# Kernel optimization log

Hardware: AMD Instinct MI355X
Metric: run time of the kernel (lower is better)

The kernel has to match this reference:

```python
import jax, jax.numpy as jnp
import numpy as np

B, L, D = 4, 2048, 128  # batch, input_dim == seq_len, memory/key/query/value dim
EPS_RMS = float(np.finfo(np.float32).eps)  # torch nn.RMSNorm default eps
EPS_NORM = 1e-12                           # F.normalize default eps


def setup_inputs() -> dict:
    key = jax.random.key(0)
    ks = jax.random.split(key, 20)
    s = 0.02
    rnd = lambda k, shape: jax.random.normal(k, shape, jnp.float32) * s
    return {
        "x": jax.random.normal(ks[0], (B, L, L), jnp.float32),
        "k_proj_w": rnd(ks[1], (D, L)), "k_proj_b": rnd(ks[2], (D,)),
        "q_proj_w": rnd(ks[3], (D, L)), "q_proj_b": rnd(ks[4], (D,)),
        "v_proj_w": rnd(ks[5], (D, L)), "v_proj_b": rnd(ks[6], (D,)),
        "k_conv_w": rnd(ks[7], (D, D, 3, 3)), "k_conv_b": rnd(ks[8], (D,)),
        "q_conv_w": rnd(ks[9], (D, D, 3, 3)), "q_conv_b": rnd(ks[10], (D,)),
        "v_conv_w": rnd(ks[11], (D, D, 3, 3)), "v_conv_b": rnd(ks[12], (D,)),
        "beta_w": rnd(ks[13], (1, L)), "beta_b": rnd(ks[14], (1,)),
        "rms_w": jnp.ones((D,), jnp.float32),
        "out_w": rnd(ks[15], (L, D)), "out_b": rnd(ks[16], (L,)),
    }


def _conv3x3(x4, w, b):
    # x4: (B, Cin, H, 1); w: (Cout, Cin, 3, 3); padding=1 both dims (torch Conv2d)
    y = jax.lax.conv_general_dilated(
        x4, w, window_strides=(1, 1), padding=((1, 1), (1, 1)),
        dimension_numbers=("NCHW", "OIHW", "NCHW"))
    return y + b[None, :, None, None]


def _l2_normalize_last(x):
    # F.normalize(p=2, dim=-1): here last dim is the SEQUENCE dim (faithful to source)
    n = jnp.sqrt(jnp.sum(x * x, axis=-1, keepdims=True))
    return x / jnp.maximum(n, EPS_NORM)


def _delta_rule(k, q, v, beta):
    # k, q, v: (B, D, L); beta: (B, L, 1)
    # S_t = S_{t-1} (I - b_t k_t k_t^T) + b_t v_t k_t^T ; o_t = S_t q_t
    kt = jnp.transpose(k, (2, 0, 1))          # (L, B, D)
    qt = jnp.transpose(q, (2, 0, 1))
    vt = jnp.transpose(v, (2, 0, 1))
    bt = jnp.transpose(beta, (1, 0, 2))       # (L, B, 1)

    S0 = jnp.zeros((k.shape[0], k.shape[1], k.shape[1]), k.dtype)

    def step(S, xs):
        k_t, q_t, v_t, b_t = xs               # (B,D),(B,D),(B,D),(B,1)
        b = b_t[:, :, None]                   # (B,1,1)
        Sk = jnp.einsum("bij,bj->bi", S, k_t)  # (B,D)
        S = S - b * (Sk[:, :, None] * k_t[:, None, :]) \
              + b * (v_t[:, :, None] * k_t[:, None, :])
        o = jnp.einsum("bij,bj->bi", S, q_t)   # (B,D)
        return S, o

    _, o = jax.lax.scan(step, S0, (kt, qt, vt, bt))
    return jnp.transpose(o, (1, 0, 2))        # (B, L, D)


def reference(x, k_proj_w, k_proj_b, q_proj_w, q_proj_b, v_proj_w, v_proj_b,
              k_conv_w, k_conv_b, q_conv_w, q_conv_b, v_conv_w, v_conv_b,
              beta_w, beta_b, rms_w, out_w, out_b):
    b_, _, sl = x.shape                       # (B, L, L); seq_len == input_dim
    k = x @ k_proj_w.T + k_proj_b             # (B, L, D)
    q = x @ q_proj_w.T + q_proj_b
    v = x @ v_proj_w.T + v_proj_b
    # torch .view on contiguous tensor = raw row-major reshape (NOT transpose)
    k = k.reshape(b_, D, sl, 1)
    q = q.reshape(b_, D, sl, 1)
    v = v.reshape(b_, D, sl, 1)
    k = _conv3x3(k, k_conv_w, k_conv_b).reshape(b_, D, sl)
    q = _conv3x3(q, q_conv_w, q_conv_b).reshape(b_, D, sl)
    v = _conv3x3(v, v_conv_w, v_conv_b).reshape(b_, D, sl)
    k, q, v = jax.nn.silu(k), jax.nn.silu(q), jax.nn.silu(v)
    k, q = _l2_normalize_last(k), _l2_normalize_last(q)
    beta = jax.nn.sigmoid(x @ beta_w.T + beta_b)      # (B, L, 1)
    delta = _delta_rule(k, q, v, beta)                # (B, L, D)
    # RMSNorm over memory_dim (last axis), affine weight
    ms = jnp.mean(delta * delta, axis=-1, keepdims=True)
    normed = delta * jax.lax.rsqrt(ms + EPS_RMS) * rms_w
    return normed @ out_w.T + out_b                   # (B, L, input_dim)
```

## Files before the change

### kernel.cpp

```cpp
#include <hip/hip_runtime.h>
#include <math.h>

#define LL 2048
#define DD 128
#define BB 4
#define CK 64
#define NCHUNK 32

typedef __bf16 bf16x8 __attribute__((ext_vector_type(8)));
typedef __bf16 bf16x4 __attribute__((ext_vector_type(4)));
typedef float floatx4 __attribute__((ext_vector_type(4)));

__global__ __launch_bounds__(256) void proj_gemm_mfma(
    const float* __restrict__ x,
    const float* __restrict__ kw, const float* __restrict__ qw, const float* __restrict__ vw,
    const float* __restrict__ kb, const float* __restrict__ qb, const float* __restrict__ vb,
    float* __restrict__ k0, float* __restrict__ q0, float* __restrict__ v0)
{
    const int arr = blockIdx.y;
    const float* __restrict__ w   = arr == 0 ? kw : (arr == 1 ? qw : vw);
    const float* __restrict__ bia = arr == 0 ? kb : (arr == 1 ? qb : vb);
    float* __restrict__ out       = arr == 0 ? k0 : (arr == 1 ? q0 : v0);

    __shared__ __bf16 As[128][72];
    __shared__ __bf16 Bs[128][72];

    const int t    = threadIdx.x;
    const int wave = t >> 6, lane = t & 63;
    const int wm   = wave & 1, wn = wave >> 1;
    const int m    = lane & 15, quad = lane >> 4;
    const int row0 = blockIdx.x * 128;

    floatx4 acc[4][4] = {};

    for (int k0i = 0; k0i < 2048; k0i += 64) {
        #pragma unroll
        for (int c = 0; c < 4; c++) {
            int chunk = t + c * 256;
            int r = chunk >> 3, p = chunk & 7;
            const float4* src = (const float4*)&x[(size_t)(row0 + r) * 2048 + k0i + p * 8];
            float4 f0 = src[0], f1 = src[1];
            bf16x8 v8;
            v8[0] = (__bf16)f0.x; v8[1] = (__bf16)f0.y; v8[2] = (__bf16)f0.z; v8[3] = (__bf16)f0.w;
            v8[4] = (__bf16)f1.x; v8[5] = (__bf16)f1.y; v8[6] = (__bf16)f1.z; v8[7] = (__bf16)f1.w;
            *(bf16x8*)&As[r][p * 8] = v8;
        }
        #pragma unroll
        for (int c = 0; c < 4; c++) {
            int chunk = t + c * 256;
            int r = chunk >> 3, p = chunk & 7;
            const float4* src = (const float4*)&w[(size_t)r * 2048 + k0i + p * 8];
            float4 f0 = src[0], f1 = src[1];
            bf16x8 v8;
            v8[0] = (__bf16)f0.x; v8[1] = (__bf16)f0.y; v8[2] = (__bf16)f0.z; v8[3] = (__bf16)f0.w;
            v8[4] = (__bf16)f1.x; v8[5] = (__bf16)f1.y; v8[6] = (__bf16)f1.z; v8[7] = (__bf16)f1.w;
            *(bf16x8*)&Bs[r][p * 8] = v8;
        }
        __syncthreads();
        #pragma unroll
        for (int ks = 0; ks < 2; ks++) {
            bf16x8 af[4], bfr[4];
            #pragma unroll
            for (int i = 0; i < 4; i++)
                af[i] = *(const bf16x8*)&As[wm * 64 + i * 16 + m][ks * 32 + quad * 8];
            #pragma unroll
            for (int j = 0; j < 4; j++)
                bfr[j] = *(const bf16x8*)&Bs[wn * 64 + j * 16 + m][ks * 32 + quad * 8];
            #pragma unroll
            for (int i = 0; i < 4; i++)
                #pragma unroll
                for (int j = 0; j < 4; j++)
                    acc[i][j] = __builtin_amdgcn_mfma_f32_16x16x32_bf16(af[i], bfr[j], acc[i][j], 0, 0, 0);
        }
        __syncthreads();
    }
    #pragma unroll
    for (int i = 0; i < 4; i++) {
        int grow = row0 + wm * 64 + i * 16 + quad * 4;
        #pragma unroll
        for (int j = 0; j < 4; j++) {
            int col = wn * 64 + j * 16 + m;
            float bv = bia[col];
            #pragma unroll
            for (int r = 0; r < 4; r++)
                out[(size_t)(grow + r) * 128 + col] = acc[i][j][r] + bv;
        }
    }
}

__global__ __launch_bounds__(256) void out_gemm_mfma(
    const __bf16* __restrict__ A, const float* __restrict__ w,
    const float* __restrict__ bias, float* __restrict__ out)
{
    __shared__ __bf16 As[128][72];
    __shared__ __bf16 Bs[128][72];

    const int t    = threadIdx.x;
    const int wave = t >> 6, lane = t & 63;
    const int wm   = wave & 1, wn = wave >> 1;
    const int m    = lane & 15, quad = lane >> 4;
    const int row0 = blockIdx.x * 128;
    const int col0 = blockIdx.y * 128;

    floatx4 acc[4][4] = {};

    for (int k0i = 0; k0i < 128; k0i += 64) {
        #pragma unroll
        for (int c = 0; c < 4; c++) {
            int chunk = t + c * 256;
            int r = chunk >> 3, p = chunk & 7;
            *(bf16x8*)&As[r][p * 8] = *(const bf16x8*)&A[(size_t)(row0 + r) * 128 + k0i + p * 8];
        }
        #pragma unroll
        for (int c = 0; c < 4; c++) {
            int chunk = t + c * 256;
            int r = chunk >> 3, p = chunk & 7;
            const float4* src = (const float4*)&w[(size_t)(col0 + r) * 128 + k0i + p * 8];
            float4 f0 = src[0], f1 = src[1];
            bf16x8 v8;
            v8[0] = (__bf16)f0.x; v8[1] = (__bf16)f0.y; v8[2] = (__bf16)f0.z; v8[3] = (__bf16)f0.w;
            v8[4] = (__bf16)f1.x; v8[5] = (__bf16)f1.y; v8[6] = (__bf16)f1.z; v8[7] = (__bf16)f1.w;
            *(bf16x8*)&Bs[r][p * 8] = v8;
        }
        __syncthreads();
        #pragma unroll
        for (int ks = 0; ks < 2; ks++) {
            bf16x8 af[4], bfr[4];
            #pragma unroll
            for (int i = 0; i < 4; i++)
                af[i] = *(const bf16x8*)&As[wm * 64 + i * 16 + m][ks * 32 + quad * 8];
            #pragma unroll
            for (int j = 0; j < 4; j++)
                bfr[j] = *(const bf16x8*)&Bs[wn * 64 + j * 16 + m][ks * 32 + quad * 8];
            #pragma unroll
            for (int i = 0; i < 4; i++)
                #pragma unroll
                for (int j = 0; j < 4; j++)
                    acc[i][j] = __builtin_amdgcn_mfma_f32_16x16x32_bf16(af[i], bfr[j], acc[i][j], 0, 0, 0);
        }
        __syncthreads();
    }
    #pragma unroll
    for (int i = 0; i < 4; i++) {
        int grow = row0 + wm * 64 + i * 16 + quad * 4;
        #pragma unroll
        for (int j = 0; j < 4; j++) {
            int col = col0 + wn * 64 + j * 16 + m;
            float bv = bias[col];
            #pragma unroll
            for (int r = 0; r < 4; r++)
                out[(size_t)(grow + r) * 2048 + col] = acc[i][j][r] + bv;
        }
    }
}

__global__ __launch_bounds__(256) void beta_kernel(
    const float* __restrict__ x, const float* __restrict__ bw,
    const float* __restrict__ bb, float* __restrict__ beta)
{
    const int row = blockIdx.x;
    const float* xr = x + (size_t)row * 2048;
    float s = 0.f;
    for (int j = threadIdx.x; j < 2048; j += 256) s = fmaf(xr[j], bw[j], s);
    #pragma unroll
    for (int m = 1; m < 64; m <<= 1) s += __shfl_xor(s, m, 64);
    __shared__ float red[4];
    if ((threadIdx.x & 63) == 0) red[threadIdx.x >> 6] = s;
    __syncthreads();
    if (threadIdx.x == 0) {
        float tot = red[0] + red[1] + red[2] + red[3] + bb[0];
        beta[row] = 1.f / (1.f + expf(-tot));
    }
}

__global__ __launch_bounds__(256) void wpack_zero(
    const float* __restrict__ kw, const float* __restrict__ qw, const float* __restrict__ vw,
    __bf16* __restrict__ wpk, float* __restrict__ sumsq)
{
    const int t = threadIdx.x;
    if (blockIdx.x == 0) {
        #pragma unroll
        for (int e = 0; e < 4; e++) sumsq[t * 4 + e] = 0.f;
    }
    int base = (blockIdx.x * 256 + t) * 4;
    int arr = base / 49152, rem = base % 49152;
    const float* __restrict__ w = arr == 0 ? kw : arr == 1 ? qw : vw;
    int dt = rem / 16384, rem2 = rem % 16384;
    int o = rem2 >> 7, i0 = rem2 & 127;
    #pragma unroll
    for (int e = 0; e < 4; e++) {
        int i = i0 + e;
        wpk[base + e] = (__bf16)w[(size_t)((o * 128 + i) * 3 + dt) * 3 + 1];
    }
}

__global__ __launch_bounds__(256) void conv_mfma(
    const float* __restrict__ k0, const float* __restrict__ q0, const float* __restrict__ v0,
    const __bf16* __restrict__ wpk,
    const float* __restrict__ kb, const float* __restrict__ qb, const float* __restrict__ vb,
    float* __restrict__ kcT, float* __restrict__ qcT, float* __restrict__ vcT,
    float* __restrict__ sumsq)
{
    const int sb  = blockIdx.x;
    const int arr = blockIdx.y >> 2;
    const int b   = blockIdx.y & 3;
    const float* __restrict__ in = (arr == 0 ? k0 : arr == 1 ? q0 : v0) + (size_t)b * DD * LL;
    const float* __restrict__ bi = arr == 0 ? kb : arr == 1 ? qb : vb;
    float* __restrict__ out      = (arr == 0 ? kcT : arr == 1 ? qcT : vcT) + (size_t)b * LL * DD;
    const __bf16* __restrict__ wp = wpk + (size_t)arr * 3 * DD * DD;

    __shared__ __bf16 Xs[66 * 136];
    __shared__ float colsum[128];

    const int t = threadIdx.x;
    const int s0 = sb * 64;
    if (t < 128) colsum[t] = 0.f;

    #pragma unroll
    for (int p = 0; p < 32; p++) {
        int idx = t + p * 256;
        int sr = idx & 63, i = idx >> 6;
        float v = in[(size_t)i * LL + s0 + sr];
        int row = sr + 1;
        Xs[row * 136 + (i ^ ((row & 7) << 4))] = (__bf16)v;
    }
    {
        int e = t >> 7, i = t & 127;
        int row = e * 65;
        int s = s0 - 1 + e * 65;
        float v = (s >= 0 && s < LL) ? in[(size_t)i * LL + s] : 0.f;
        Xs[row * 136 + (i ^ ((row & 7) << 4))] = (__bf16)v;
    }
    __syncthreads();

    const int wave = t >> 6, lane = t & 63;
    const int wm = wave & 1, wn = wave >> 1;
    const int m = lane & 15, quad = lane >> 4;

    floatx4 acc[2][4] = {};
    #pragma unroll
    for (int dt = 0; dt < 3; dt++) {
        bf16x8 bfr[4][4];
        #pragma unroll
        for (int ks = 0; ks < 4; ks++)
            #pragma unroll
            for (int j = 0; j < 4; j++)
                bfr[ks][j] = *(const bf16x8*)&wp[(size_t)(dt * DD + wn * 64 + j * 16 + m) * DD + ks * 32 + quad * 8];
        #pragma unroll
        for (int ks = 0; ks < 4; ks++) {
            bf16x8 af[2];
            #pragma unroll
            for (int ii = 0; ii < 2; ii++) {
                int row = wm * 32 + ii * 16 + m + dt;
                af[ii] = *(const bf16x8*)&Xs[row * 136 + ((ks * 32 + quad * 8) ^ ((row & 7) << 4))];
            }
            #pragma unroll
            for (int ii = 0; ii < 2; ii++)
                #pragma unroll
                for (int j = 0; j < 4; j++)
                    acc[ii][j] = __builtin_amdgcn_mfma_f32_16x16x32_bf16(af[ii], bfr[ks][j], acc[ii][j], 0, 0, 0);
        }
    }

    float part[4] = {0.f, 0.f, 0.f, 0.f};
    #pragma unroll
    for (int ii = 0; ii < 2; ii++)
        #pragma unroll
        for (int j = 0; j < 4; j++) {
            int col = wn * 64 + j * 16 + m;
            float bv = bi[col];
            #pragma unroll
            for (int r = 0; r < 4; r++) {
                int srow = s0 + wm * 32 + ii * 16 + quad * 4 + r;
                float v = acc[ii][j][r] + bv;
                float y = v / (1.f + expf(-v));
                out[(size_t)srow * DD + col] = y;
                part[j] = fmaf(y, y, part[j]);
            }
        }
    if (arr < 2) {
        #pragma unroll
        for (int j = 0; j < 4; j++)
            atomicAdd(&colsum[wn * 64 + j * 16 + m], part[j]);
        __syncthreads();
        if (t < 128) atomicAdd(&sumsq[arr * 512 + b * 128 + t], colsum[t]);
    }
}


__global__ __launch_bounds__(256) void chunk_pre1(
    const float* __restrict__ kTg, const float* __restrict__ qTg, const float* __restrict__ vTg,
    const float* __restrict__ beta, const float* __restrict__ sumsq,
    __bf16* __restrict__ Lb, __bf16* __restrict__ Wb, __bf16* __restrict__ Ub)
{
    const int c = blockIdx.x, b = blockIdx.y;
    const int gc = b * NCHUNK + c;
    const int t0 = c * CK;
    const float* kbase = kTg + ((size_t)b * LL + t0) * DD;
    const float* qbase = qTg + ((size_t)b * LL + t0) * DD;
    const float* vbase = vTg + ((size_t)b * LL + t0) * DD;

    __shared__ __bf16 Ks[CK][136];
    __shared__ __bf16 Qs[CK][136];
    __shared__ float  Af[CK][65];
    __shared__ float  WU[CK][257];
    __shared__ float  betas[CK];

    const int t = threadIdx.x;
    #pragma unroll
    for (int p = 0; p < 8; p++) {
        int idx = t + p * 256;
        int r = idx >> 5, c4 = idx & 31;
        float4 sk = *(const float4*)&sumsq[b * 128 + c4 * 4];
        float4 sq = *(const float4*)&sumsq[512 + b * 128 + c4 * 4];
        float ik0 = rsqrtf(fmaxf(sk.x, 1e-24f)), ik1 = rsqrtf(fmaxf(sk.y, 1e-24f));
        float ik2 = rsqrtf(fmaxf(sk.z, 1e-24f)), ik3 = rsqrtf(fmaxf(sk.w, 1e-24f));
        float iq0 = rsqrtf(fmaxf(sq.x, 1e-24f)), iq1 = rsqrtf(fmaxf(sq.y, 1e-24f));
        float iq2 = rsqrtf(fmaxf(sq.z, 1e-24f)), iq3 = rsqrtf(fmaxf(sq.w, 1e-24f));
        float4 f = *(const float4*)&kbase[(size_t)r * DD + c4 * 4];
        bf16x4 v; v[0] = (__bf16)(f.x * ik0); v[1] = (__bf16)(f.y * ik1);
        v[2] = (__bf16)(f.z * ik2); v[3] = (__bf16)(f.w * ik3);
        *(bf16x4*)&Ks[r][c4 * 4] = v;
        float4 g = *(const float4*)&qbase[(size_t)r * DD + c4 * 4];
        bf16x4 u; u[0] = (__bf16)(g.x * iq0); u[1] = (__bf16)(g.y * iq1);
        u[2] = (__bf16)(g.z * iq2); u[3] = (__bf16)(g.w * iq3);
        *(bf16x4*)&Qs[r][c4 * 4] = u;
    }
    if (t < CK) betas[t] = beta[(size_t)b * LL + t0 + t];
    __syncthreads();

    const int wave = t >> 6, lane = t & 63;
    const int wm = wave & 1, wn = wave >> 1;
    const int m = lane & 15, quad = lane >> 4;

    floatx4 accM[2][2] = {}, accL[2][2] = {};
    #pragma unroll
    for (int ks = 0; ks < 4; ks++) {
        bf16x8 ak[2], aq[2], bk[2];
        #pragma unroll
        for (int i = 0; i < 2; i++) {
            ak[i] = *(const bf16x8*)&Ks[wm * 32 + i * 16 + m][ks * 32 + quad * 8];
            aq[i] = *(const bf16x8*)&Qs[wm * 32 + i * 16 + m][ks * 32 + quad * 8];
            bk[i] = *(const bf16x8*)&Ks[wn * 32 + i * 16 + m][ks * 32 + quad * 8];
        }
        #pragma unroll
        for (int i = 0; i < 2; i++)
            #pragma unroll
            for (int j = 0; j < 2; j++) {
                accM[i][j] = __builtin_amdgcn_mfma_f32_16x16x32_bf16(ak[i], bk[j], accM[i][j], 0, 0, 0);
                accL[i][j] = __builtin_amdgcn_mfma_f32_16x16x32_bf16(aq[i], bk[j], accL[i][j], 0, 0, 0);
            }
    }
    #pragma unroll
    for (int i = 0; i < 2; i++)
        #pragma unroll
        for (int j = 0; j < 2; j++)
            #pragma unroll
            for (int r = 0; r < 4; r++) {
                int row = wm * 32 + i * 16 + quad * 4 + r;
                int col = wn * 32 + j * 16 + m;
                Af[row][col] = (col < row) ? betas[row] * accM[i][j][r] : 0.f;
                Lb[((size_t)gc * CK + row) * CK + col] =
                    (col <= row) ? (__bf16)accL[i][j][r] : (__bf16)0.f;
            }
    __syncthreads();

    const int col = t;
    const float* rbase = (col < DD) ? kbase : vbase;
    const int cm = col & (DD - 1);
    const float scale = (col < DD) ? rsqrtf(fmaxf(sumsq[b * 128 + cm], 1e-24f)) : 1.f;
    float cur = rbase[cm] * scale;
    for (int tt = 0; tt < CK; tt++) {
        float nxt = (tt < CK - 1) ? rbase[(size_t)(tt + 1) * DD + cm] * scale : 0.f;
        float acc = betas[tt] * cur;
        for (int s = 0; s < tt; s++)
            acc -= Af[tt][s] * WU[s][col];
        WU[tt][col] = acc;
        __bf16 bv = (__bf16)acc;
        if (col < DD) Wb[((size_t)gc * CK + tt) * DD + col] = bv;
        else          Ub[((size_t)gc * CK + tt) * DD + cm]  = bv;
        cur = nxt;
    }
}

__global__ __launch_bounds__(256) void chunk_pre2(
    const float* __restrict__ kTg, const float* __restrict__ qTg,
    const float* __restrict__ sumsq,
    const __bf16* __restrict__ Lb, const __bf16* __restrict__ Wb, const __bf16* __restrict__ Ub,
    __bf16* __restrict__ HTb, __bf16* __restrict__ Gb,
    __bf16* __restrict__ Pb, __bf16* __restrict__ Yb)
{
    const int c = blockIdx.x, b = blockIdx.y;
    const int gc = b * NCHUNK + c;
    const int t0 = c * CK;

    __shared__ __bf16 Kt[DD][72];
    __shared__ __bf16 Wt[DD][72];
    __shared__ __bf16 Ut[DD][72];
    __shared__ __bf16 Ls[CK][72];

    const int t = threadIdx.x;
    #pragma unroll
    for (int p = 0; p < 8; p++) {
        int idx = t + p * 256;
        int tt = idx >> 5, j4 = idx & 31;
        float4 sk = *(const float4*)&sumsq[b * 128 + j4 * 4];
        float4 f = *(const float4*)&kTg[((size_t)b * LL + t0 + tt) * DD + j4 * 4];
        Kt[j4 * 4 + 0][tt] = (__bf16)(f.x * rsqrtf(fmaxf(sk.x, 1e-24f)));
        Kt[j4 * 4 + 1][tt] = (__bf16)(f.y * rsqrtf(fmaxf(sk.y, 1e-24f)));
        Kt[j4 * 4 + 2][tt] = (__bf16)(f.z * rsqrtf(fmaxf(sk.z, 1e-24f)));
        Kt[j4 * 4 + 3][tt] = (__bf16)(f.w * rsqrtf(fmaxf(sk.w, 1e-24f)));
        bf16x4 w = *(const bf16x4*)&Wb[((size_t)gc * CK + tt) * DD + j4 * 4];
        bf16x4 u = *(const bf16x4*)&Ub[((size_t)gc * CK + tt) * DD + j4 * 4];
        #pragma unroll
        for (int e = 0; e < 4; e++) { Wt[j4 * 4 + e][tt] = w[e]; Ut[j4 * 4 + e][tt] = u[e]; }
    }
    #pragma unroll
    for (int p = 0; p < 4; p++) {
        int idx = t + p * 256;
        int tt = idx >> 4, s4 = idx & 15;
        *(bf16x4*)&Ls[tt][s4 * 4] = *(const bf16x4*)&Lb[((size_t)gc * CK + tt) * CK + s4 * 4];
    }
    __syncthreads();

    const int wave = t >> 6, lane = t & 63;
    const int wm = wave & 1, wn = wave >> 1;
    const int m = lane & 15, quad = lane >> 4;

    {
        floatx4 acc[4][4] = {};
        #pragma unroll
        for (int ks = 0; ks < 2; ks++) {
            bf16x8 a[4], bb[4];
            #pragma unroll
            for (int i = 0; i < 4; i++) {
                a[i]  = *(const bf16x8*)&Kt[wm * 64 + i * 16 + m][ks * 32 + quad * 8];
                bb[i] = *(const bf16x8*)&Wt[wn * 64 + i * 16 + m][ks * 32 + quad * 8];
            }
            #pragma unroll
            for (int i = 0; i < 4; i++)
                #pragma unroll
                for (int j = 0; j < 4; j++)
                    acc[i][j] = __builtin_amdgcn_mfma_f32_16x16x32_bf16(a[i], bb[j], acc[i][j], 0, 0, 0);
        }
        #pragma unroll
        for (int i = 0; i < 4; i++)
            #pragma unroll
            for (int j = 0; j < 4; j++)
                #pragma unroll
                for (int r = 0; r < 4; r++) {
                    int row = wm * 64 + i * 16 + quad * 4 + r;
                    int cx  = wn * 64 + j * 16 + m;
                    HTb[((size_t)gc * DD + row) * DD + cx] = (__bf16)(-acc[i][j][r]);
                }
    }
    {
        floatx4 acc[4][4] = {};
        #pragma unroll
        for (int ks = 0; ks < 2; ks++) {
            bf16x8 a[4], bb[4];
            #pragma unroll
            for (int i = 0; i < 4; i++) {
                a[i]  = *(const bf16x8*)&Ut[wm * 64 + i * 16 + m][ks * 32 + quad * 8];
                bb[i] = *(const bf16x8*)&Kt[wn * 64 + i * 16 + m][ks * 32 + quad * 8];
            }
            #pragma unroll
            for (int i = 0; i < 4; i++)
                #pragma unroll
                for (int j = 0; j < 4; j++)
                    acc[i][j] = __builtin_amdgcn_mfma_f32_16x16x32_bf16(a[i], bb[j], acc[i][j], 0, 0, 0);
        }
        #pragma unroll
        for (int i = 0; i < 4; i++)
            #pragma unroll
            for (int j = 0; j < 4; j++)
                #pragma unroll
                for (int r = 0; r < 4; r++) {
                    int row = wm * 64 + i * 16 + quad * 4 + r;
                    int cx  = wn * 64 + j * 16 + m;
                    Gb[((size_t)gc * DD + row) * DD + cx] = (__bf16)acc[i][j][r];
                }
    }
    {
        floatx4 acc[2][4] = {};
        #pragma unroll
        for (int ks = 0; ks < 2; ks++) {
            bf16x8 a[2], bb[4];
            #pragma unroll
            for (int i = 0; i < 2; i++)
                a[i] = *(const bf16x8*)&Ls[wm * 32 + i * 16 + m][ks * 32 + quad * 8];
            #pragma unroll
            for (int j = 0; j < 4; j++)
                bb[j] = *(const bf16x8*)&Wt[wn * 64 + j * 16 + m][ks * 32 + quad * 8];
            #pragma unroll
            for (int i = 0; i < 2; i++)
                #pragma unroll
                for (int j = 0; j < 4; j++)
                    acc[i][j] = __builtin_amdgcn_mfma_f32_16x16x32_bf16(a[i], bb[j], acc[i][j], 0, 0, 0);
        }
        #pragma unroll
        for (int i = 0; i < 2; i++)
            #pragma unroll
            for (int j = 0; j < 4; j++)
                #pragma unroll
                for (int r = 0; r < 4; r++) {
                    int row = wm * 32 + i * 16 + quad * 4 + r;
                    int cx  = wn * 64 + j * 16 + m;
                    float iq = rsqrtf(fmaxf(sumsq[512 + b * 128 + cx], 1e-24f));
                    float qv = qTg[((size_t)b * LL + t0 + row) * DD + cx] * iq;
                    Pb[((size_t)gc * CK + row) * DD + cx] = (__bf16)(qv - acc[i][j][r]);
                }
    }
    {
        floatx4 acc[2][4] = {};
        #pragma unroll
        for (int ks = 0; ks < 2; ks++) {
            bf16x8 a[2], bb[4];
            #pragma unroll
            for (int i = 0; i < 2; i++)
                a[i] = *(const bf16x8*)&Ls[wm * 32 + i * 16 + m][ks * 32 + quad * 8];
            #pragma unroll
            for (int j = 0; j < 4; j++)
                bb[j] = *(const bf16x8*)&Ut[wn * 64 + j * 16 + m][ks * 32 + quad * 8];
            #pragma unroll
            for (int i = 0; i < 2; i++)
                #pragma unroll
                for (int j = 0; j < 4; j++)
                    acc[i][j] = __builtin_amdgcn_mfma_f32_16x16x32_bf16(a[i], bb[j], acc[i][j], 0, 0, 0);
        }
        #pragma unroll
        for (int i = 0; i < 2; i++)
            #pragma unroll
            for (int j = 0; j < 4; j++)
                #pragma unroll
                for (int r = 0; r < 4; r++) {
                    int row = wm * 32 + i * 16 + quad * 4 + r;
                    int cx  = wn * 64 + j * 16 + m;
                    Yb[((size_t)gc * CK + row) * DD + cx] = (__bf16)acc[i][j][r];
                }
    }
}

__global__ __launch_bounds__(256) void delta_serial(
    const __bf16* __restrict__ HTb, const __bf16* __restrict__ Gb, __bf16* __restrict__ S0b)
{
    const int b  = blockIdx.x >> 2;
    const int rg = blockIdx.x & 3;
    __shared__ __bf16 Ss[32][136];
    const int t = threadIdx.x;
    const int wj = t >> 6;
    const int lane = t & 63;
    const int m = lane & 15, quad = lane >> 4;

    floatx4 acc[2][2] = {};
    bf16x8 hA[8], hB[8];
    __bf16 gpre[16];

    {
        const size_t g0 = (size_t)(b * NCHUNK) * DD * DD;
        #pragma unroll
        for (int ks = 0; ks < 4; ks++)
            #pragma unroll
            for (int j = 0; j < 2; j++) {
                int hr = wj * 32 + j * 16 + m;
                hA[ks * 2 + j] = *(const bf16x8*)&HTb[g0 + (size_t)hr * DD + ks * 32 + quad * 8];
            }
        #pragma unroll
        for (int i = 0; i < 2; i++)
            #pragma unroll
            for (int j = 0; j < 2; j++)
                #pragma unroll
                for (int r = 0; r < 4; r++) {
                    int row = rg * 32 + i * 16 + quad * 4 + r;
                    int cx  = wj * 32 + j * 16 + m;
                    gpre[(i * 2 + j) * 4 + r] = Gb[g0 + (size_t)row * DD + cx];
                }
    }

    for (int c = 0; c < NCHUNK; c++) {
        const size_t gco = (size_t)(b * NCHUNK + c) * DD * DD;
        const size_t gcn = gco + (size_t)DD * DD;
        const bool even = (c & 1) == 0;
        if (c + 1 < NCHUNK) {
            #pragma unroll
            for (int ks = 0; ks < 4; ks++)
                #pragma unroll
                for (int j = 0; j < 2; j++) {
                    int hr = wj * 32 + j * 16 + m;
                    bf16x8 v = *(const bf16x8*)&HTb[gcn + (size_t)hr * DD + ks * 32 + quad * 8];
                    if (even) hB[ks * 2 + j] = v; else hA[ks * 2 + j] = v;
                }
        }
        #pragma unroll
        for (int i = 0; i < 2; i++)
            #pragma unroll
            for (int j = 0; j < 2; j++) {
                int row = i * 16 + quad * 4;
                int cx  = wj * 32 + j * 16 + m;
                #pragma unroll
                for (int r = 0; r < 4; r++)
                    Ss[row + r][cx] = (__bf16)acc[i][j][r];
            }
        __syncthreads();
        #pragma unroll
        for (int p = 0; p < 4; p++) {
            int idx = t + p * 256;
            int row = idx >> 5, c4 = idx & 31;
            *(bf16x4*)&S0b[gco + (size_t)(rg * 32 + row) * DD + c4 * 4] =
                *(const bf16x4*)&Ss[row][c4 * 4];
        }
        #pragma unroll
        for (int i = 0; i < 2; i++)
            #pragma unroll
            for (int j = 0; j < 2; j++)
                #pragma unroll
                for (int r = 0; r < 4; r++)
                    acc[i][j][r] += (float)gpre[(i * 2 + j) * 4 + r];
        if (c + 1 < NCHUNK) {
            #pragma unroll
            for (int i = 0; i < 2; i++)
                #pragma unroll
                for (int j = 0; j < 2; j++)
                    #pragma unroll
                    for (int r = 0; r < 4; r++) {
                        int row = rg * 32 + i * 16 + quad * 4 + r;
                        int cx  = wj * 32 + j * 16 + m;
                        gpre[(i * 2 + j) * 4 + r] = Gb[gcn + (size_t)row * DD + cx];
                    }
        }
        #pragma unroll
        for (int ks = 0; ks < 4; ks++) {
            bf16x8 a[2];
            #pragma unroll
            for (int i = 0; i < 2; i++)
                a[i] = *(const bf16x8*)&Ss[i * 16 + m][ks * 32 + quad * 8];
            #pragma unroll
            for (int i = 0; i < 2; i++)
                #pragma unroll
                for (int j = 0; j < 2; j++) {
                    bf16x8 hb = even ? hA[ks * 2 + j] : hB[ks * 2 + j];
                    acc[i][j] = __builtin_amdgcn_mfma_f32_16x16x32_bf16(a[i], hb, acc[i][j], 0, 0, 0);
                }
        }
        __syncthreads();
    }
}

__global__ __launch_bounds__(256) void chunk_out(
    const __bf16* __restrict__ Pb, const __bf16* __restrict__ Yb, const __bf16* __restrict__ S0b,
    const float* __restrict__ rms_w, __bf16* __restrict__ nmb)
{
    const int c = blockIdx.x, b = blockIdx.y;
    const int gc = b * NCHUNK + c;
    const int t0 = c * CK;
    __shared__ __bf16 Ps[CK][136];
    __shared__ __bf16 Sb[DD][136];
    __shared__ float red[2][2][2][4][4];
    const int t = threadIdx.x;
    #pragma unroll
    for (int p = 0; p < 8; p++) {
        int idx = t + p * 256;
        int row = idx >> 5, c4 = idx & 31;
        *(bf16x4*)&Ps[row][c4 * 4] = *(const bf16x4*)&Pb[((size_t)gc * CK + row) * DD + c4 * 4];
    }
    #pragma unroll
    for (int p = 0; p < 16; p++) {
        int idx = t + p * 256;
        int row = idx >> 5, c4 = idx & 31;
        *(bf16x4*)&Sb[row][c4 * 4] = *(const bf16x4*)&S0b[((size_t)gc * DD + row) * DD + c4 * 4];
    }
    __syncthreads();

    const int wave = t >> 6, lane = t & 63;
    const int wm = wave & 1, wn = wave >> 1;
    const int m = lane & 15, quad = lane >> 4;

    floatx4 acc[2][4] = {};
    #pragma unroll
    for (int ks = 0; ks < 4; ks++) {
        bf16x8 a[2], bb[4];
        #pragma unroll
        for (int i = 0; i < 2; i++)
            a[i] = *(const bf16x8*)&Ps[wm * 32 + i * 16 + m][ks * 32 + quad * 8];
        #pragma unroll
        for (int j = 0; j < 4; j++)
            bb[j] = *(const bf16x8*)&Sb[wn * 64 + j * 16 + m][ks * 32 + quad * 8];
        #pragma unroll
        for (int i = 0; i < 2; i++)
            #pragma unroll
            for (int j = 0; j < 4; j++)
                acc[i][j] = __builtin_amdgcn_mfma_f32_16x16x32_bf16(a[i], bb[j], acc[i][j], 0, 0, 0);
    }

    float v[2][4][4];
    float ss[2][4] = {};
    #pragma unroll
    for (int i = 0; i < 2; i++)
        #pragma unroll
        for (int j = 0; j < 4; j++)
            #pragma unroll
            for (int r = 0; r < 4; r++) {
                int row = wm * 32 + i * 16 + quad * 4 + r;
                int cx  = wn * 64 + j * 16 + m;
                float y = (float)Yb[((size_t)gc * CK + row) * DD + cx];
                float vv = acc[i][j][r] + y;
                v[i][j][r] = vv;
                ss[i][r] = fmaf(vv, vv, ss[i][r]);
            }
    #pragma unroll
    for (int mask = 1; mask < 16; mask <<= 1)
        #pragma unroll
        for (int i = 0; i < 2; i++)
            #pragma unroll
            for (int r = 0; r < 4; r++)
                ss[i][r] += __shfl_xor(ss[i][r], mask, 64);
    if (m == 0)
        #pragma unroll
        for (int i = 0; i < 2; i++)
            #pragma unroll
            for (int r = 0; r < 4; r++)
                red[wn][wm][i][quad][r] = ss[i][r];
    __syncthreads();
    #pragma unroll
    for (int i = 0; i < 2; i++)
        #pragma unroll
        for (int r = 0; r < 4; r++) {
            float tot = red[0][wm][i][quad][r] + red[1][wm][i][quad][r];
            float inv = rsqrtf(tot * (1.f / 128.f) + 1.1920928955078125e-07f);
            int row = wm * 32 + i * 16 + quad * 4 + r;
            #pragma unroll
            for (int j = 0; j < 4; j++) {
                int cx = wn * 64 + j * 16 + m;
                nmb[((size_t)b * LL + t0 + row) * DD + cx] = (__bf16)(v[i][j][r] * inv * rms_w[cx]);
            }
        }
}

extern "C" void kernel_launch(void* const* d_in, const int* in_sizes, int n_in,
                              void* d_out, int out_size, void* d_ws, size_t ws_size,
                              hipStream_t stream) {
    const float* x    = (const float*)d_in[0];
    const float* kpw  = (const float*)d_in[1];
    const float* kpb  = (const float*)d_in[2];
    const float* qpw  = (const float*)d_in[3];
    const float* qpb  = (const float*)d_in[4];
    const float* vpw  = (const float*)d_in[5];
    const float* vpb  = (const float*)d_in[6];
    const float* kcw  = (const float*)d_in[7];
    const float* kcb  = (const float*)d_in[8];
    const float* qcw  = (const float*)d_in[9];
    const float* qcb  = (const float*)d_in[10];
    const float* vcw  = (const float*)d_in[11];
    const float* vcb  = (const float*)d_in[12];
    const float* bw   = (const float*)d_in[13];
    const float* bb   = (const float*)d_in[14];
    const float* rw   = (const float*)d_in[15];
    const float* ow   = (const float*)d_in[16];
    const float* obi  = (const float*)d_in[17];
    float* out = (float*)d_out;

    float* ws = (float*)d_ws;
    const size_t NB1 = (size_t)BB * DD * LL;
    float* k0  = ws;
    float* q0  = ws + NB1;
    float* v0  = ws + 2 * NB1;
    float* kcT = ws + 3 * NB1;
    float* qcT = ws + 4 * NB1;
    float* vcT = ws + 5 * NB1;
    float* beta  = ws + 8 * NB1;
    float* sumsq = beta + (size_t)BB * LL;
    __bf16* wpk  = (__bf16*)(sumsq + 1024);

    __bf16* Lb  = (__bf16*)k0;
    __bf16* Wb  = Lb + (size_t)128 * 64 * 64;
    __bf16* Ub  = (__bf16*)q0;
    __bf16* HTb = (__bf16*)v0;
    __bf16* Gb  = (__bf16*)vcT;
    __bf16* Pb  = (__bf16*)(ws + 7 * NB1);
    __bf16* Yb  = Pb + (size_t)128 * 64 * 128;
    __bf16* S0b = (__bf16*)k0;
    __bf16* nmb = (__bf16*)(ws + 6 * NB1);

    proj_gemm_mfma<<<dim3(64, 3), 256, 0, stream>>>(x, kpw, qpw, vpw, kpb, qpb, vpb, k0, q0, v0);
    beta_kernel<<<dim3(BB * LL), 256, 0, stream>>>(x, bw, bb, beta);
    wpack_zero<<<dim3(144), 256, 0, stream>>>(kcw, qcw, vcw, wpk, sumsq);
    conv_mfma<<<dim3(32, 12), 256, 0, stream>>>(k0, q0, v0, wpk, kcb, qcb, vcb, kcT, qcT, vcT, sumsq);
    chunk_pre1<<<dim3(NCHUNK, BB), 256, 0, stream>>>(kcT, qcT, vcT, beta, sumsq, Lb, Wb, Ub);
    chunk_pre2<<<dim3(NCHUNK, BB), 256, 0, stream>>>(kcT, qcT, sumsq, Lb, Wb, Ub, HTb, Gb, Pb, Yb);
    delta_serial<<<dim3(BB * 4), 256, 0, stream>>>(HTb, Gb, S0b);
    chunk_out<<<dim3(NCHUNK, BB), 256, 0, stream>>>(Pb, Yb, S0b, rw, nmb);
    out_gemm_mfma<<<dim3(64, 16), 256, 0, stream>>>(nmb, ow, obi, out);
}
```

Before: 364.6 us.

## Pre-convert x and weights to bf16, double-buffer projection GEMM with direct-to-LDS loads

The beta kernel now also writes a bf16 copy of x into the output buffer, which serves as scratch. The weight-pack kernel converts the projection and output weights to bf16 once. The projection GEMM reads these bf16 operands with global_load_lds into double-buffered shared memory, using 64-row tiles to launch more blocks. The output GEMM loads its full K=128 tile in one pass. The aim is to remove repeated fp32-to-bf16 conversion inside the GEMM inner loops and to overlap loads with MFMA work. The cost is an extra bf16 write and read of x. The unpadded LDS layout may also cause bank conflicts.

```diff
diff --git a/kernel.cpp b/kernel.cpp
--- a/kernel.cpp
+++ b/kernel.cpp
@@ -11,63 +11,71 @@
 typedef __bf16 bf16x4 __attribute__((ext_vector_type(4)));
 typedef float floatx4 __attribute__((ext_vector_type(4)));
 
+__device__ __forceinline__ void gload_lds16(const void* g, void* l) {
+    __builtin_amdgcn_global_load_lds(
+        (const __attribute__((address_space(1))) unsigned int*)g,
+        (__attribute__((address_space(3))) unsigned int*)l, 16, 0, 0);
+}
+
 __global__ __launch_bounds__(256) void proj_gemm_mfma(
-    const float* __restrict__ x,
-    const float* __restrict__ kw, const float* __restrict__ qw, const float* __restrict__ vw,
+    const __bf16* __restrict__ xb, const __bf16* __restrict__ wcat,
     const float* __restrict__ kb, const float* __restrict__ qb, const float* __restrict__ vb,
     float* __restrict__ k0, float* __restrict__ q0, float* __restrict__ v0)
 {
     const int arr = blockIdx.y;
-    const float* __restrict__ w   = arr == 0 ? kw : (arr == 1 ? qw : vw);
     const float* __restrict__ bia = arr == 0 ? kb : (arr == 1 ? qb : vb);
     float* __restrict__ out       = arr == 0 ? k0 : (arr == 1 ? q0 : v0);
-
-    __shared__ __bf16 As[128][72];
-    __shared__ __bf16 Bs[128][72];
-
-    const int t    = threadIdx.x;
+    const __bf16* __restrict__ w  = wcat + (size_t)arr * DD * 2048;
+
+    __shared__ __bf16 As[2][64 * 64];
+    __shared__ __bf16 Bs[2][128 * 64];
+
+    const int t = threadIdx.x;
     const int wave = t >> 6, lane = t & 63;
-    const int wm   = wave & 1, wn = wave >> 1;
-    const int m    = lane & 15, quad = lane >> 4;
-    const int row0 = blockIdx.x * 128;
-
-    floatx4 acc[4][4] = {};
-
-    for (int k0i = 0; k0i < 2048; k0i += 64) {
-        #pragma unroll
-        for (int c = 0; c < 4; c++) {
-            int chunk = t + c * 256;
-            int r = chunk >> 3, p = chunk & 7;
-            const float4* src = (const float4*)&x[(size_t)(row0 + r) * 2048 + k0i + p * 8];
-            float4 f0 = src[0], f1 = src[1];
-            bf16x8 v8;
-            v8[0] = (__bf16)f0.x; v8[1] = (__bf16)f0.y; v8[2] = (__bf16)f0.z; v8[3] = (__bf16)f0.w;
-            v8[4] = (__bf16)f1.x; v8[5] = (__bf16)f1.y; v8[6] = (__bf16)f1.z; v8[7] = (__bf16)f1.w;
-            *(bf16x8*)&As[r][p * 8] = v8;
-        }
-        #pragma unroll
-        for (int c = 0; c < 4; c++) {
-            int chunk = t + c * 256;
-            int r = chunk >> 3, p = chunk & 7;
-            const float4* src = (const float4*)&w[(size_t)r * 2048 + k0i + p * 8];
-            float4 f0 = src[0], f1 = src[1];
-            bf16x8 v8;
-            v8[0] = (__bf16)f0.x; v8[1] = (__bf16)f0.y; v8[2] = (__bf16)f0.z; v8[3] = (__bf16)f0.w;
-            v8[4] = (__bf16)f1.x; v8[5] = (__bf16)f1.y; v8[6] = (__bf16)f1.z; v8[7] = (__bf16)f1.w;
-            *(bf16x8*)&Bs[r][p * 8] = v8;
-        }
-        __syncthreads();
+    const int wm = wave & 1, wn = wave >> 1;
+    const int m = lane & 15, quad = lane >> 4;
+    const int row0 = blockIdx.x * 64;
+
+    floatx4 acc[2][4] = {};
+
+    #pragma unroll
+    for (int c = 0; c < 2; c++) {
+        int f = t + c * 256;
+        gload_lds16(&xb[(size_t)(row0 + (f >> 3)) * 2048 + (f & 7) * 8], &As[0][f * 8]);
+    }
+    #pragma unroll
+    for (int c = 0; c < 4; c++) {
+        int f = t + c * 256;
+        gload_lds16(&w[(size_t)(f >> 3) * 2048 + (f & 7) * 8], &Bs[0][f * 8]);
+    }
+    __syncthreads();
+
+    for (int kt = 0; kt < 32; kt++) {
+        const int cur = kt & 1, nxt = cur ^ 1;
+        if (kt + 1 < 32) {
+            const int k0i = (kt + 1) * 64;
+            #pragma unroll
+            for (int c = 0; c < 2; c++) {
+                int f = t + c * 256;
+                gload_lds16(&xb[(size_t)(row0 + (f >> 3)) * 2048 + k0i + (f & 7) * 8], &As[nxt][f * 8]);
+            }
+            #pragma unroll
+            for (int c = 0; c < 4; c++) {
+                int f = t + c * 256;
+                gload_lds16(&w[(size_t)(f >> 3) * 2048 + k0i + (f & 7) * 8], &Bs[nxt][f * 8]);
+            }
+        }
         #pragma unroll
         for (int ks = 0; ks < 2; ks++) {
-            bf16x8 af[4], bfr[4];
-            #pragma unroll
-            for (int i = 0; i < 4; i++)
-                af[i] = *(const bf16x8*)&As[wm * 64 + i * 16 + m][ks * 32 + quad * 8];
-            #pragma unroll
-            for (int j = 0; j < 4; j++)
-                bfr[j] = *(const bf16x8*)&Bs[wn * 64 + j * 16 + m][ks * 32 + quad * 8];
-            #pragma unroll
-            for (int i = 0; i < 4; i++)
+            bf16x8 af[2], bfr[4];
+            #pragma unroll
+            for (int i = 0; i < 2; i++)
+                af[i] = *(const bf16x8*)&As[cur][(wm * 32 + i * 16 + m) * 64 + ks * 32 + quad * 8];
+            #pragma unroll
+            for (int j = 0; j < 4; j++)
+                bfr[j] = *(const bf16x8*)&Bs[cur][(wn * 64 + j * 16 + m) * 64 + ks * 32 + quad * 8];
+            #pragma unroll
+            for (int i = 0; i < 2; i++)
                 #pragma unroll
                 for (int j = 0; j < 4; j++)
                     acc[i][j] = __builtin_amdgcn_mfma_f32_16x16x32_bf16(af[i], bfr[j], acc[i][j], 0, 0, 0);
@@ -75,70 +83,54 @@
         __syncthreads();
     }
     #pragma unroll
-    for (int i = 0; i < 4; i++) {
-        int grow = row0 + wm * 64 + i * 16 + quad * 4;
+    for (int i = 0; i < 2; i++)
         #pragma unroll
         for (int j = 0; j < 4; j++) {
             int col = wn * 64 + j * 16 + m;
             float bv = bia[col];
             #pragma unroll
             for (int r = 0; r < 4; r++)
-                out[(size_t)(grow + r) * 128 + col] = acc[i][j][r] + bv;
-        }
-    }
+                out[(size_t)(row0 + wm * 32 + i * 16 + quad * 4 + r) * 128 + col] = acc[i][j][r] + bv;
+        }
 }
 
 __global__ __launch_bounds__(256) void out_gemm_mfma(
-    const __bf16* __restrict__ A, const float* __restrict__ w,
+    const __bf16* __restrict__ A, const __bf16* __restrict__ wb,
     const float* __restrict__ bias, float* __restrict__ out)
 {
-    __shared__ __bf16 As[128][72];
-    __shared__ __bf16 Bs[128][72];
-
-    const int t    = threadIdx.x;
+    __shared__ __bf16 As[128 * 128];
+    __shared__ __bf16 Bs[128 * 128];
+
+    const int t = threadIdx.x;
     const int wave = t >> 6, lane = t & 63;
-    const int wm   = wave & 1, wn = wave >> 1;
-    const int m    = lane & 15, quad = lane >> 4;
+    const int wm = wave & 1, wn = wave >> 1;
+    const int m = lane & 15, quad = lane >> 4;
     const int row0 = blockIdx.x * 128;
     const int col0 = blockIdx.y * 128;
 
+    #pragma unroll
+    for (int c = 0; c < 8; c++) {
+        int f = t + c * 256;
+        gload_lds16(&A[(size_t)(row0 + (f >> 4)) * 128 + (f & 15) * 8], &As[f * 8]);
+        gload_lds16(&wb[(size_t)(col0 + (f >> 4)) * 128 + (f & 15) * 8], &Bs[f * 8]);
+    }
+    __syncthreads();
+
     floatx4 acc[4][4] = {};
-
-    for (int k0i = 0; k0i < 128; k0i += 64) {
-        #pragma unroll
-        for (int c = 0; c < 4; c++) {
-            int chunk = t + c * 256;
-            int r = chunk >> 3, p = chunk & 7;
-            *(bf16x8*)&As[r][p * 8] = *(const bf16x8*)&A[(size_t)(row0 + r) * 128 + k0i + p * 8];
-        }
-        #pragma unroll
-        for (int c = 0; c < 4; c++) {
-            int chunk = t + c * 256;
-            int r = chunk >> 3, p = chunk & 7;
-            const float4* src = (const float4*)&w[(size_t)(col0 + r) * 128 + k0i + p * 8];
-            float4 f0 = src[0], f1 = src[1];
-            bf16x8 v8;
-            v8[0] = (__bf16)f0.x; v8[1] = (__bf16)f0.y; v8[2] = (__bf16)f0.z; v8[3] = (__bf16)f0.w;
-            v8[4] = (__bf16)f1.x; v8[5] = (__bf16)f1.y; v8[6] = (__bf16)f1.z; v8[7] = (__bf16)f1.w;
-            *(bf16x8*)&Bs[r][p * 8] = v8;
-        }
-        __syncthreads();
-        #pragma unroll
-        for (int ks = 0; ks < 2; ks++) {
-            bf16x8 af[4], bfr[4];
-            #pragma unroll
-            for (int i = 0; i < 4; i++)
-                af[i] = *(const bf16x8*)&As[wm * 64 + i * 16 + m][ks * 32 + quad * 8];
-            #pragma unroll
-            for (int j = 0; j < 4; j++)
-                bfr[j] = *(const bf16x8*)&Bs[wn * 64 + j * 16 + m][ks * 32 + quad * 8];
-            #pragma unroll
-            for (int i = 0; i < 4; i++)
-                #pragma unroll
-                for (int j = 0; j < 4; j++)
-                    acc[i][j] = __builtin_amdgcn_mfma_f32_16x16x32_bf16(af[i], bfr[j], acc[i][j], 0, 0, 0);
-        }
-        __syncthreads();
+    #pragma unroll
+    for (int ks = 0; ks < 4; ks++) {
+        bf16x8 af[4], bfr[4];
+        #pragma unroll
+        for (int i = 0; i < 4; i++)
+            af[i] = *(const bf16x8*)&As[(wm * 64 + i * 16 + m) * 128 + ks * 32 + quad * 8];
+        #pragma unroll
+        for (int j = 0; j < 4; j++)
+            bfr[j] = *(const bf16x8*)&Bs[(wn * 64 + j * 16 + m) * 128 + ks * 32 + quad * 8];
+        #pragma unroll
+        for (int i = 0; i < 4; i++)
+            #pragma unroll
+            for (int j = 0; j < 4; j++)
+                acc[i][j] = __builtin_amdgcn_mfma_f32_16x16x32_bf16(af[i], bfr[j], acc[i][j], 0, 0, 0);
     }
     #pragma unroll
     for (int i = 0; i < 4; i++) {
@@ -156,18 +148,29 @@
 
 __global__ __launch_bounds__(256) void beta_kernel(
     const float* __restrict__ x, const float* __restrict__ bw,
-    const float* __restrict__ bb, float* __restrict__ beta)
+    const float* __restrict__ bb, float* __restrict__ beta, __bf16* __restrict__ xb)
 {
     const int row = blockIdx.x;
     const float* xr = x + (size_t)row * 2048;
+    __bf16* xbr = xb + (size_t)row * 2048;
+    const int t = threadIdx.x;
     float s = 0.f;
-    for (int j = threadIdx.x; j < 2048; j += 256) s = fmaf(xr[j], bw[j], s);
+    #pragma unroll
+    for (int jj = 0; jj < 2; jj++) {
+        int j = (t + jj * 256) * 4;
+        float4 f = *(const float4*)&xr[j];
+        float4 wv = *(const float4*)&bw[j];
+        s = fmaf(f.x, wv.x, s); s = fmaf(f.y, wv.y, s);
+        s = fmaf(f.z, wv.z, s); s = fmaf(f.w, wv.w, s);
+        bf16x4 v; v[0] = (__bf16)f.x; v[1] = (__bf16)f.y; v[2] = (__bf16)f.z; v[3] = (__bf16)f.w;
+        *(bf16x4*)&xbr[j] = v;
+    }
     #pragma unroll
     for (int m = 1; m < 64; m <<= 1) s += __shfl_xor(s, m, 64);
     __shared__ float red[4];
-    if ((threadIdx.x & 63) == 0) red[threadIdx.x >> 6] = s;
+    if ((t & 63) == 0) red[t >> 6] = s;
     __syncthreads();
-    if (threadIdx.x == 0) {
+    if (t == 0) {
         float tot = red[0] + red[1] + red[2] + red[3] + bb[0];
         beta[row] = 1.f / (1.f + expf(-tot));
     }
@@ -175,22 +178,40 @@
 
 __global__ __launch_bounds__(256) void wpack_zero(
     const float* __restrict__ kw, const float* __restrict__ qw, const float* __restrict__ vw,
-    __bf16* __restrict__ wpk, float* __restrict__ sumsq)
+    const float* __restrict__ kpw, const float* __restrict__ qpw, const float* __restrict__ vpw,
+    const float* __restrict__ ow,
+    __bf16* __restrict__ wpk, __bf16* __restrict__ wcat, __bf16* __restrict__ owb,
+    float* __restrict__ sumsq)
 {
     const int t = threadIdx.x;
-    if (blockIdx.x == 0) {
+    const int bx = blockIdx.x;
+    if (bx == 0) {
         #pragma unroll
         for (int e = 0; e < 4; e++) sumsq[t * 4 + e] = 0.f;
     }
-    int base = (blockIdx.x * 256 + t) * 4;
-    int arr = base / 49152, rem = base % 49152;
-    const float* __restrict__ w = arr == 0 ? kw : arr == 1 ? qw : vw;
-    int dt = rem / 16384, rem2 = rem % 16384;
-    int o = rem2 >> 7, i0 = rem2 & 127;
-    #pragma unroll
-    for (int e = 0; e < 4; e++) {
-        int i = i0 + e;
-        wpk[base + e] = (__bf16)w[(size_t)((o * 128 + i) * 3 + dt) * 3 + 1];
+    if (bx < 144) {
+        int base = (bx * 256 + t) * 4;
+        int arr = base / 49152, rem = base % 49152;
+        const float* __restrict__ w = arr == 0 ? kw : arr == 1 ? qw : vw;
+        int dt = rem / 16384, rem2 = rem % 16384;
+        int o = rem2 >> 7, i0 = rem2 & 127;
+        #pragma unroll
+        for (int e = 0; e < 4; e++) {
+            int i = i0 + e;
+            wpk[base + e] = (__bf16)w[(size_t)((o * 128 + i) * 3 + dt) * 3 + 1];
+        }
+    } else if (bx < 912) {
+        int e = (bx - 144) * 1024 + t * 4;
+        int arr = e >> 18, rem = e & 262143;
+        const float* __restrict__ w = arr == 0 ? kpw : arr == 1 ? qpw : vpw;
+        float4 f = *(const float4*)&w[rem];
+        bf16x4 v; v[0] = (__bf16)f.x; v[1] = (__bf16)f.y; v[2] = (__bf16)f.z; v[3] = (__bf16)f.w;
+        *(bf16x4*)&wcat[(size_t)arr * 262144 + rem] = v;
+    } else {
+        int e = (bx - 912) * 1024 + t * 4;
+        float4 f = *(const float4*)&ow[e];
+        bf16x4 v; v[0] = (__bf16)f.x; v[1] = (__bf16)f.y; v[2] = (__bf16)f.z; v[3] = (__bf16)f.w;
+        *(bf16x4*)&owb[e] = v;
     }
 }
 
@@ -770,6 +791,8 @@
     float* beta  = ws + 8 * NB1;
     float* sumsq = beta + (size_t)BB * LL;
     __bf16* wpk  = (__bf16*)(sumsq + 1024);
+    __bf16* wcat = wpk + (size_t)147456;
+    __bf16* owb  = wcat + (size_t)786432;
 
     __bf16* Lb  = (__bf16*)k0;
     __bf16* Wb  = Lb + (size_t)128 * 64 * 64;
@@ -780,14 +803,15 @@
     __bf16* Yb  = Pb + (size_t)128 * 64 * 128;
     __bf16* S0b = (__bf16*)k0;
     __bf16* nmb = (__bf16*)(ws + 6 * NB1);
-
-    proj_gemm_mfma<<<dim3(64, 3), 256, 0, stream>>>(x, kpw, qpw, vpw, kpb, qpb, vpb, k0, q0, v0);
-    beta_kernel<<<dim3(BB * LL), 256, 0, stream>>>(x, bw, bb, beta);
-    wpack_zero<<<dim3(144), 256, 0, stream>>>(kcw, qcw, vcw, wpk, sumsq);
+    __bf16* xb  = (__bf16*)d_out;
+
+    wpack_zero<<<dim3(1168), 256, 0, stream>>>(kcw, qcw, vcw, kpw, qpw, vpw, ow, wpk, wcat, owb, sumsq);
+    beta_kernel<<<dim3(BB * LL), 256, 0, stream>>>(x, bw, bb, beta, xb);
+    proj_gemm_mfma<<<dim3(128, 3), 256, 0, stream>>>(xb, wcat, kpb, qpb, vpb, k0, q0, v0);
     conv_mfma<<<dim3(32, 12), 256, 0, stream>>>(k0, q0, v0, wpk, kcb, qcb, vcb, kcT, qcT, vcT, sumsq);
     chunk_pre1<<<dim3(NCHUNK, BB), 256, 0, stream>>>(kcT, qcT, vcT, beta, sumsq, Lb, Wb, Ub);
     chunk_pre2<<<dim3(NCHUNK, BB), 256, 0, stream>>>(kcT, qcT, sumsq, Lb, Wb, Ub, HTb, Gb, Pb, Yb);
     delta_serial<<<dim3(BB * 4), 256, 0, stream>>>(HTb, Gb, S0b);
     chunk_out<<<dim3(NCHUNK, BB), 256, 0, stream>>>(Pb, Yb, S0b, rw, nmb);
-    out_gemm_mfma<<<dim3(64, 16), 256, 0, stream>>>(nmb, ow, obi, out);
-}
+    out_gemm_mfma<<<dim3(64, 16), 256, 0, stream>>>(nmb, owb, obi, out);
+}
```

Result: faster. 349.8 us (-4.1%).
